# Performance work log

Measured on AMD Instinct MI355X. Metric: run time of the kernel, lower is better.

Reference implementation:

```python
import jax, jax.numpy as jnp
import numpy as np

B, T, C = 16, 512, 1024   # batch, frames, activation_dim
D = 4096                  # dict_size
K = 128                   # top-k per window
WIN = 8                   # window_size


def setup_inputs() -> dict:
    key = jax.random.key(0)
    k1, k2, k3, k4 = jax.random.split(key, 4)
    # decoder weight (C, D), columns normalized as in __init__
    W_dec = jax.random.normal(k1, (C, D), jnp.float32)
    W_dec = W_dec / jnp.linalg.norm(W_dec, axis=0, keepdims=True)
    # encoder initialized as decoder transpose (then independently perturbed to mimic training)
    W_enc = W_dec.T + 0.01 * jax.random.normal(k2, (D, C), jnp.float32)
    b_enc = 0.01 * jax.random.normal(k3, (D,), jnp.float32)
    b_dec = 0.01 * jax.random.normal(k4, (C,), jnp.float32)
    x = jax.random.normal(jax.random.fold_in(key, 7), (B, T, C), jnp.float32)
    return {"x": x, "W_enc": W_enc, "b_enc": b_enc, "W_dec": W_dec, "b_dec": b_dec}


def _window_topk(pre, k, win):
    # pre: (B, T, D) post-relu activations
    b, t, d = pre.shape
    pad = (-t) % win  # static
    if pad:
        pre_p = jnp.pad(pre, ((0, 0), (0, pad), (0, 0)))
    else:
        pre_p = pre
    tp = t + pad
    nw = tp // win
    xw = pre_p.reshape(b, nw, win, d)
    ws = xw.sum(axis=2)                        # (B, nw, D) window sums
    _, idx = jax.lax.top_k(ws, k)              # (B, nw, K)
    # scatter 1.0 at top-k dictionary entries per (batch, window) row
    idx_flat = idx.reshape(b * nw, k)
    rows = jnp.arange(b * nw)[:, None]
    mask = jnp.zeros((b * nw, d), pre.dtype).at[rows, idx_flat].set(1.0)
    mask = mask.reshape(b, nw, 1, d)
    sparse = (xw * mask).reshape(b, tp, d)[:, :t]
    return sparse


def reference(x, W_enc, b_enc, W_dec, b_dec):
    # encode: relu((x - b_dec) @ W_enc^T + b_enc)
    pre = jax.nn.relu(jnp.einsum('btc,dc->btd', x - b_dec, W_enc) + b_enc)  # (B,T,D)
    encoded = _window_topk(pre, K, WIN)                                     # (B,T,D)
    # decode: encoded @ W_dec^T + b_dec
    recon = jnp.einsum('btd,cd->btc', encoded, W_dec) + b_dec               # (B,T,C)
    return recon, encoded
```

## Files before the change

kernel.cpp:

```cpp
#include <hip/hip_runtime.h>

#define B_   16
#define T_   512
#define C_   1024
#define D_   4096
#define K_   128
#define WIN_ 8
#define NW_  (T_ / WIN_)
#define M_   (B_ * T_)

typedef __attribute__((ext_vector_type(8))) short bf16x8_t;
typedef __attribute__((ext_vector_type(4))) float f32x4_t;

__device__ __forceinline__ void gload16(const void* g, void* l) {
    __builtin_amdgcn_global_load_lds(
        (const __attribute__((address_space(1))) void*)g,
        (__attribute__((address_space(3))) void*)l, 16, 0, 0);
}

__device__ __forceinline__ unsigned short f2bf(float f) {
    unsigned u = __float_as_uint(f);
    unsigned r = (u + 0x7fffu + ((u >> 16) & 1u)) >> 16;
    return (unsigned short)r;
}
__device__ __forceinline__ float bf2f(unsigned short h) {
    return __uint_as_float((unsigned)h << 16);
}

__device__ __forceinline__ unsigned f2key(float f) {
    unsigned u = __float_as_uint(f);
    return (u & 0x80000000u) ? ~u : (u | 0x80000000u);
}
__device__ __forceinline__ float key2f(unsigned k) {
    unsigned u = (k & 0x80000000u) ? (k & 0x7fffffffu) : ~k;
    return __uint_as_float(u);
}

__global__ __launch_bounds__(256) void prep_cvt_wenc(
    const float* __restrict__ W_enc, const float* __restrict__ b_enc,
    const float* __restrict__ b_dec, unsigned short* __restrict__ wencbf,
    float* __restrict__ benc2)
{
    int d = blockIdx.x;
    int tid = threadIdx.x;
    float4 wv = ((const float4*)(W_enc + (size_t)d * C_))[tid];
    uint2 o;
    o.x = (unsigned)f2bf(wv.x) | ((unsigned)f2bf(wv.y) << 16);
    o.y = (unsigned)f2bf(wv.z) | ((unsigned)f2bf(wv.w) << 16);
    ((uint2*)(wencbf + (size_t)d * C_))[tid] = o;
    float4 bv = ((const float4*)b_dec)[tid];
    float s = wv.x * bv.x + wv.y * bv.y + wv.z * bv.z + wv.w * bv.w;
    __shared__ float red[256];
    red[tid] = s;
    __syncthreads();
    for (int off = 128; off > 0; off >>= 1) {
        if (tid < off) red[tid] += red[tid + off];
        __syncthreads();
    }
    if (tid == 0) benc2[d] = b_enc[d] - red[0];
}

__global__ void cvt_bf16(const float* __restrict__ in, unsigned short* __restrict__ out, int n8)
{
    int i = blockIdx.x * blockDim.x + threadIdx.x;
    if (i >= n8) return;
    const float4* p = (const float4*)(in + (size_t)i * 8);
    float4 a = p[0], b = p[1];
    uint4 o;
    o.x = (unsigned)f2bf(a.x) | ((unsigned)f2bf(a.y) << 16);
    o.y = (unsigned)f2bf(a.z) | ((unsigned)f2bf(a.w) << 16);
    o.z = (unsigned)f2bf(b.x) | ((unsigned)f2bf(b.y) << 16);
    o.w = (unsigned)f2bf(b.z) | ((unsigned)f2bf(b.w) << 16);
    ((uint4*)out)[i] = o;
}

__global__ void transpose_wdec(const float* __restrict__ W, unsigned short* __restrict__ WT)
{
    __shared__ float tile[32][33];
    int d0 = blockIdx.x * 32;
    int c0 = blockIdx.y * 32;
    int tx = threadIdx.x, ty = threadIdx.y;
    #pragma unroll
    for (int i = 0; i < 32; i += 8)
        tile[ty + i][tx] = W[(size_t)(c0 + ty + i) * D_ + d0 + tx];
    __syncthreads();
    #pragma unroll
    for (int i = 0; i < 32; i += 8)
        WT[(size_t)(d0 + ty + i) * C_ + c0 + tx] = f2bf(tile[tx][ty + i]);
}

__global__ __launch_bounds__(256) void mfma_gemm_dense(
    const unsigned short* __restrict__ Abf,
    const unsigned short* __restrict__ Bbf,
    const float* __restrict__ benc2,
    float* __restrict__ enc,
    float* __restrict__ wsums)
{
    __shared__ unsigned short lA[128 * 32];
    __shared__ unsigned short lB[128 * 32];
    __shared__ float cst[4][16][68];
    int tid = threadIdx.x;
    int lane = tid & 63;
    int wv = tid >> 6;
    int wm = wv >> 1, wn = wv & 1;

    int lid = blockIdx.y * gridDim.x + blockIdx.x;
    int sw = (lid & 7) * 256 + (lid >> 3);
    int bn = sw & 31, bm = sw >> 5;

    f32x4_t acc[4][4];
    #pragma unroll
    for (int i = 0; i < 4; i++)
        #pragma unroll
        for (int j = 0; j < 4; j++) acc[i][j] = (f32x4_t){0.f, 0.f, 0.f, 0.f};

    const unsigned short* Ab = Abf + (size_t)bm * 128 * C_;
    const unsigned short* Bb = Bbf + (size_t)bn * 128 * C_;

    int m_s[2], u_s[2];
    #pragma unroll
    for (int q = 0; q < 2; q++) {
        int p = q * 256 + tid;
        int m = p >> 2, v = p & 3;
        m_s[q] = m;
        u_s[q] = v ^ ((m >> 1) & 3);
    }

    int r = lane & 15, g = lane >> 4;
    for (int k0 = 0; k0 < C_; k0 += 32) {
        __syncthreads();
        #pragma unroll
        for (int q = 0; q < 2; q++) {
            gload16(Ab + (size_t)m_s[q] * C_ + k0 + u_s[q] * 8,
                    &lA[(q * 256 + wv * 64) * 8]);
            gload16(Bb + (size_t)m_s[q] * C_ + k0 + u_s[q] * 8,
                    &lB[(q * 256 + wv * 64) * 8]);
        }
        __syncthreads();
        bf16x8_t af[4], bfr[4];
        #pragma unroll
        for (int mi = 0; mi < 4; mi++) {
            int m = wm * 64 + mi * 16 + r;
            int u = g ^ ((m >> 1) & 3);
            af[mi] = *(const bf16x8_t*)&lA[m * 32 + u * 8];
        }
        #pragma unroll
        for (int ni = 0; ni < 4; ni++) {
            int d = wn * 64 + ni * 16 + r;
            int u = g ^ ((d >> 1) & 3);
            bfr[ni] = *(const bf16x8_t*)&lB[d * 32 + u * 8];
        }
        #pragma unroll
        for (int mi = 0; mi < 4; mi++)
            #pragma unroll
            for (int ni = 0; ni < 4; ni++)
                acc[mi][ni] = __builtin_amdgcn_mfma_f32_16x16x32_bf16(
                    af[mi], bfr[ni], acc[mi][ni], 0, 0, 0);
    }

    int b = bm >> 2;
    int t_blk = (bm & 3) * 128;
    int dbase = bn * 128 + wn * 64;
    int mbase_w = bm * 128 + wm * 64;
    int wbase = b * NW_ + (t_blk >> 3) + wm * 8;

    float bias_r[4];
    #pragma unroll
    for (int ni = 0; ni < 4; ni++) bias_r[ni] = benc2[dbase + ni * 16 + r];

    float wsv[4][4];
    #pragma unroll
    for (int mi = 0; mi < 4; mi++) {
        #pragma unroll
        for (int ni = 0; ni < 4; ni++) {
            float s = 0.f;
            #pragma unroll
            for (int q = 0; q < 4; q++) {
                float v = acc[mi][ni][q] + bias_r[ni];
                v = v > 0.f ? v : 0.f;
                cst[wv][g * 4 + q][ni * 16 + r] = v;
                s += v;
            }
            float partner = __shfl_xor(s, 16);
            wsv[mi][ni] = s + partner;
        }
        #pragma unroll
        for (int ri = 0; ri < 4; ri++) {
            int row = ri * 4 + (lane >> 4);
            int c4 = (lane & 15) * 4;
            float4 vv = *(const float4*)&cst[wv][row][c4];
            *(float4*)(enc + (size_t)(mbase_w + mi * 16 + row) * D_ + dbase + c4) = vv;
        }
    }

    if ((g & 1) == 0) {
        #pragma unroll
        for (int mi = 0; mi < 4; mi++)
            #pragma unroll
            for (int ni = 0; ni < 4; ni++)
                cst[wv][mi * 2 + (g >> 1)][ni * 16 + r] = wsv[mi][ni];
    }
    #pragma unroll
    for (int it = 0; it < 2; it++) {
        int row = lane >> 3;
        int c4 = (lane & 7) * 4 + it * 32;
        float4 vv = *(const float4*)&cst[wv][row][c4];
        *(float4*)(wsums + (size_t)(wbase + row) * D_ + dbase + c4) = vv;
    }
}

__device__ __forceinline__ void find_bucket(
    const int* hist, int need, int shift, unsigned pref,
    unsigned* shp, int* shn, int tid)
{
    if (tid < 64) {
        int L = tid;
        int h0 = hist[L * 4], h1 = hist[L * 4 + 1];
        int h2 = hist[L * 4 + 2], h3 = hist[L * 4 + 3];
        int s3 = h3, s2 = h2 + s3, s1 = h1 + s2, s0 = h0 + s1;
        int T = s0, I = T;
        #pragma unroll
        for (int off = 1; off < 64; off <<= 1) {
            int t = __shfl_down(I, off);
            if (L + off < 64) I += t;
        }
        int H = I - T;
        int S[5] = {H + s0, H + s1, H + s2, H + s3, H};
        #pragma unroll
        for (int j = 0; j < 4; j++) {
            if (S[j] >= need && S[j + 1] < need) {
                *shp = pref | ((unsigned)(L * 4 + j) << shift);
                *shn = need - S[j + 1];
            }
        }
    }
    __syncthreads();
}

__device__ __forceinline__ void radix_select(
    const unsigned* keys, int n, int need0, int npass, unsigned maxkey,
    int* hist, unsigned* shp, int* shn, int tid)
{
    if (tid == 0) { *shp = 0u; *shn = need0; }
    __syncthreads();
    for (int pass = 0; pass < npass; ++pass) {
        int shift = 24 - pass * 8;
        unsigned pref = *shp;
        int need = *shn;
        unsigned pmask = (pass == 0) ? 0u : (0xFFFFFFFFu << (shift + 8));
        hist[tid] = 0;
        __syncthreads();
        for (int i = tid; i < n; i += 256) {
            unsigned k = keys[i];
            if (k <= maxkey && (k & pmask) == pref)
                atomicAdd(&hist[(k >> shift) & 0xFF], 1);
        }
        __syncthreads();
        find_bucket(hist, need, shift, pref, shp, shn, tid);
    }
}

__device__ __forceinline__ int block_prefix_excl(int v, int* wsum, int tid)
{
    __syncthreads();
    int lane = tid & 63, wv = tid >> 6;
    int x = v;
    #pragma unroll
    for (int off = 1; off < 64; off <<= 1) {
        int t = __shfl_up(x, off);
        if (lane >= off) x += t;
    }
    if (lane == 63) wsum[wv] = x;
    __syncthreads();
    int base = 0;
    #pragma unroll
    for (int w2 = 0; w2 < 3; w2++) if (w2 < wv) base += wsum[w2];
    return base + x - v;
}

#define DELTA 0.15f
#define MAXCAND 320

__global__ __launch_bounds__(256) void fixup_topk(
    const float* __restrict__ wsums, const float* __restrict__ x,
    const float* __restrict__ W_enc, const float* __restrict__ benc2,
    unsigned* __restrict__ bmask, int* __restrict__ idxlist)
{
    int row = blockIdx.x;
    int b = row / NW_, w = row % NW_;
    int t0g = b * T_ + w * WIN_;
    __shared__ unsigned keys[D_];
    __shared__ float xs[WIN_][C_];
    __shared__ int hist[256];
    __shared__ int wsum[4];
    __shared__ unsigned sh_prefix;
    __shared__ int sh_need;
    __shared__ int cand[MAXCAND];
    __shared__ unsigned ckeys[MAXCAND];
    __shared__ int sh_ncand, sh_nhi;
    unsigned short* hbits = (unsigned short*)hist;
    int* whist = (int*)xs;
    int tid = threadIdx.x;

    for (int i = tid; i < D_ / 4; i += 256) {
        float4 v = ((const float4*)(wsums + (size_t)row * D_))[i];
        keys[i * 4 + 0] = f2key(v.x);
        keys[i * 4 + 1] = f2key(v.y);
        keys[i * 4 + 2] = f2key(v.z);
        keys[i * 4 + 3] = f2key(v.w);
    }
    for (int i = tid; i < 1024; i += 256) whist[i] = 0;
    if (tid == 0) { sh_ncand = 0; sh_nhi = 0; }
    __syncthreads();

    {
        int* myh = whist + (tid >> 6) * 256;
        for (int i = tid; i < D_; i += 256)
            atomicAdd(&myh[keys[i] >> 24], 1);
        __syncthreads();
        hist[tid] = whist[tid] + whist[256 + tid] + whist[512 + tid] + whist[768 + tid];
        __syncthreads();
        find_bucket(hist, K_, 24, 0u, &sh_prefix, &sh_need, tid);
    }
    for (int pass = 1; pass < 3; ++pass) {
        int shift = 24 - pass * 8;
        unsigned pref = sh_prefix;
        int need = sh_need;
        unsigned pmask = 0xFFFFFFFFu << (shift + 8);
        hist[tid] = 0;
        __syncthreads();
        for (int i = tid; i < D_; i += 256) {
            unsigned k = keys[i];
            if ((k & pmask) == pref)
                atomicAdd(&hist[(k >> shift) & 0xFF], 1);
        }
        __syncthreads();
        find_bucket(hist, need, shift, pref, &sh_prefix, &sh_need, tid);
    }
    float kthf = key2f(sh_prefix);
    unsigned TH_HI = f2key(kthf + DELTA);
    unsigned TH_LO = f2key(kthf - DELTA);

    for (int i = tid; i < WIN_ * C_ / 4; i += 256)
        ((float4*)xs)[i] = ((const float4*)(x + (size_t)t0g * C_))[i];
    {
        int myhi = 0;
        for (int i = tid; i < D_; i += 256) {
            unsigned k = keys[i];
            if (k > TH_HI) myhi++;
            else if (k >= TH_LO) {
                int pos = atomicAdd(&sh_ncand, 1);
                if (pos < MAXCAND) cand[pos] = i;
            }
        }
        if (myhi) atomicAdd(&sh_nhi, myhi);
    }
    __syncthreads();
    int nc = sh_ncand < MAXCAND ? sh_ncand : MAXCAND;

    {
        int wvi = tid >> 6, ln = tid & 63;
        int c0 = ln * 4;
        for (int cb = wvi; cb < nc; cb += 4) {
            int d = cand[cb];
            const float* wrow = W_enc + (size_t)d * C_;
            float a[WIN_] = {0.f, 0.f, 0.f, 0.f, 0.f, 0.f, 0.f, 0.f};
            #pragma unroll
            for (int q = 0; q < 4; q++) {
                float4 wq = *(const float4*)(wrow + q * 256 + c0);
                #pragma unroll
                for (int j = 0; j < WIN_; j++) {
                    float4 xq = *(const float4*)(&xs[j][q * 256 + c0]);
                    a[j] = fmaf(wq.x, xq.x, a[j]);
                    a[j] = fmaf(wq.y, xq.y, a[j]);
                    a[j] = fmaf(wq.z, xq.z, a[j]);
                    a[j] = fmaf(wq.w, xq.w, a[j]);
                }
            }
            #pragma unroll
            for (int off = 1; off < 64; off <<= 1)
                #pragma unroll
                for (int j = 0; j < WIN_; j++) a[j] += __shfl_xor(a[j], off);
            if (ln == 0) {
                float bias = benc2[d], s = 0.f;
                #pragma unroll
                for (int j = 0; j < WIN_; j++) {
                    float v = a[j] + bias;
                    s += v > 0.f ? v : 0.f;
                }
                unsigned k1 = f2key(s);
                keys[d] = k1;
                ckeys[cb] = k1;
            }
        }
    }
    __syncthreads();

    for (int i = tid; i < nc; i += 256)
        if (ckeys[i] > TH_HI) atomicAdd(&sh_nhi, 1);
    __syncthreads();
    int need0 = K_ - sh_nhi;
    if (need0 > 0)
        radix_select(ckeys, nc, need0, 4, TH_HI, hist, &sh_prefix, &sh_need, tid);
    else
        radix_select(keys, D_, K_, 4, 0xFFFFFFFFu, hist, &sh_prefix, &sh_need, tid);
    unsigned kth = sh_prefix;
    int need_eq = sh_need;

    int base16 = tid * 16;
    unsigned mybits = 0;
    int eqcnt = 0;
    #pragma unroll
    for (int j = 0; j < 16; ++j) {
        unsigned k = keys[base16 + j];
        if (k > kth) mybits |= (1u << j);
        else if (k == kth) eqcnt++;
    }
    int rr = block_prefix_excl(eqcnt, wsum, tid);
    #pragma unroll
    for (int j = 0; j < 16; ++j) {
        unsigned k = keys[base16 + j];
        if (k == kth) { if (rr < need_eq) mybits |= (1u << j); rr++; }
    }
    hbits[tid] = (unsigned short)mybits;
    __syncthreads();
    if (tid < D_ / 32)
        bmask[(size_t)row * (D_ / 32) + tid] =
            (unsigned)hbits[2 * tid] | ((unsigned)hbits[2 * tid + 1] << 16);

    int pos = block_prefix_excl(__popc(mybits), wsum, tid);
    #pragma unroll
    for (int j = 0; j < 16; ++j) {
        if (mybits & (1u << j)) idxlist[(size_t)row * K_ + pos++] = base16 + j;
    }
}

__global__ void apply_mask(float* __restrict__ enc, const unsigned* __restrict__ bmask)
{
    size_t idx = ((size_t)blockIdx.x * blockDim.x + threadIdx.x) * 4;
    size_t m = idx >> 12;
    int d = (int)(idx & (D_ - 1));
    int b = (int)(m / T_);
    int t = (int)(m % T_);
    int wrow = b * NW_ + (t >> 3);
    unsigned word = bmask[(size_t)wrow * (D_ / 32) + (d >> 5)];
    unsigned nib = (word >> (d & 31)) & 0xFu;
    float4 v = {0.f, 0.f, 0.f, 0.f};
    if (nib) {
        v = *(float4*)(enc + idx);
        if (!(nib & 1u)) v.x = 0.f;
        if (!(nib & 2u)) v.y = 0.f;
        if (!(nib & 4u)) v.z = 0.f;
        if (!(nib & 8u)) v.w = 0.f;
    }
    *(float4*)(enc + idx) = v;
}

__global__ __launch_bounds__(256) void decode_win(
    const float* __restrict__ enc,
    const int* __restrict__ idxlist,
    const unsigned short* __restrict__ WdTb,
    const float* __restrict__ b_dec,
    float* __restrict__ recon)
{
    int row = blockIdx.x;
    int b = row / NW_, w = row % NW_;
    int t0 = b * T_ + w * WIN_;
    __shared__ int sidx[K_];
    __shared__ float act[K_][12];
    int tid = threadIdx.x;
    if (tid < K_) sidx[tid] = idxlist[(size_t)row * K_ + tid];
    __syncthreads();
    {
        int ci = tid >> 1;
        int j4 = (tid & 1) * 4;
        int dd = sidx[ci];
        #pragma unroll
        for (int j = 0; j < 4; j++)
            act[ci][j4 + j] = enc[(size_t)(t0 + j4 + j) * D_ + dd];
    }
    __syncthreads();

    float accv[WIN_][4] = {};
    int c0 = tid * 4;
    for (int i = 0; i < K_; ++i) {
        int d = sidx[i];
        ushort4 wu = *(const ushort4*)(WdTb + (size_t)d * C_ + c0);
        float4 wv = {bf2f(wu.x), bf2f(wu.y), bf2f(wu.z), bf2f(wu.w)};
        float4 a03 = *(const float4*)(&act[i][0]);
        float4 a47 = *(const float4*)(&act[i][4]);
        float aj[8] = {a03.x, a03.y, a03.z, a03.w, a47.x, a47.y, a47.z, a47.w};
        #pragma unroll
        for (int j = 0; j < WIN_; j++) {
            accv[j][0] = fmaf(aj[j], wv.x, accv[j][0]);
            accv[j][1] = fmaf(aj[j], wv.y, accv[j][1]);
            accv[j][2] = fmaf(aj[j], wv.z, accv[j][2]);
            accv[j][3] = fmaf(aj[j], wv.w, accv[j][3]);
        }
    }
    float4 bd = *(const float4*)(b_dec + c0);
    #pragma unroll
    for (int j = 0; j < WIN_; j++) {
        float4 o;
        o.x = accv[j][0] + bd.x; o.y = accv[j][1] + bd.y;
        o.z = accv[j][2] + bd.z; o.w = accv[j][3] + bd.w;
        *(float4*)(recon + (size_t)(t0 + j) * C_ + c0) = o;
    }
}

extern "C" void kernel_launch(void* const* d_in, const int* in_sizes, int n_in,
                              void* d_out, int out_size, void* d_ws, size_t ws_size,
                              hipStream_t stream)
{
    const float* x     = (const float*)d_in[0];
    const float* W_enc = (const float*)d_in[1];
    const float* b_enc = (const float*)d_in[2];
    const float* W_dec = (const float*)d_in[3];
    const float* b_dec = (const float*)d_in[4];

    float* out   = (float*)d_out;
    float* recon = out;
    float* enc   = out + (size_t)M_ * C_;

    unsigned short* xbf   = (unsigned short*)recon;
    float*          wsums = (float*)((char*)recon + (size_t)M_ * C_ * 2);

    char* ws = (char*)d_ws;
    unsigned short* WdTb    = (unsigned short*)ws;
    unsigned*       bmask   = (unsigned*)(ws + (size_t)D_ * C_ * 4);
    int*            idxlist = (int*)((char*)bmask + (size_t)(B_ * NW_) * (D_ / 32) * 4);
    float*          benc2   = (float*)((char*)idxlist + (size_t)(B_ * NW_) * K_ * 4);
    unsigned short* wencbf  = (unsigned short*)((char*)benc2 + D_ * 4);

    prep_cvt_wenc<<<D_, 256, 0, stream>>>(W_enc, b_enc, b_dec, wencbf, benc2);
    cvt_bf16<<<(M_ * C_ / 8 + 255) / 256, 256, 0, stream>>>(x, xbf, M_ * C_ / 8);
    transpose_wdec<<<dim3(D_ / 32, C_ / 32), dim3(32, 8), 0, stream>>>(W_dec, WdTb);
    mfma_gemm_dense<<<dim3(32, 64), 256, 0, stream>>>(xbf, wencbf, benc2, enc, wsums);
    fixup_topk<<<B_ * NW_, 256, 0, stream>>>(wsums, x, W_enc, benc2, bmask, idxlist);
    apply_mask<<<(int)((size_t)M_ * D_ / 4 / 256), 256, 0, stream>>>(enc, bmask);
    decode_win<<<B_ * NW_, 256, 0, stream>>>(enc, idxlist, WdTb, b_dec, recon);
}
```

Baseline: 275.4 us.

## Fuse top-k fixup, mask application and window decode into one kernel

Merges the top-k selection, the dense mask-apply pass and the per-window decoder into a single per-window kernel. The bitmask and index list now stay in LDS instead of going through global memory, and the kept activations are gathered into LDS while the encoded rows are masked, which removes two launches and a re-read of the sparse values. The catch is that only 1024 blocks of 256 threads do the whole 128 MB enc read/write pass, which may limit memory bandwidth, and LDS regions are reused across phases.

```diff
diff --git a/kernel.cpp b/kernel.cpp
--- a/kernel.cpp
+++ b/kernel.cpp
@@ -281,10 +281,11 @@
 #define DELTA 0.15f
 #define MAXCAND 320
 
-__global__ __launch_bounds__(256) void fixup_topk(
+__global__ __launch_bounds__(256) void fixup_mask_decode(
     const float* __restrict__ wsums, const float* __restrict__ x,
     const float* __restrict__ W_enc, const float* __restrict__ benc2,
-    unsigned* __restrict__ bmask, int* __restrict__ idxlist)
+    const unsigned short* __restrict__ WdTb, const float* __restrict__ b_dec,
+    float* __restrict__ enc, float* __restrict__ recon)
 {
     int row = blockIdx.x;
     int b = row / NW_, w = row % NW_;
@@ -300,6 +301,10 @@
     __shared__ int sh_ncand, sh_nhi;
     unsigned short* hbits = (unsigned short*)hist;
     int* whist = (int*)xs;
+    float (*act)[12] = (float(*)[12])xs;
+    int*      sidx      = cand;
+    unsigned* bmask_lds = (unsigned*)(cand + 128);
+    int*      pprefix   = (int*)ckeys;
     int tid = threadIdx.x;
 
     for (int i = tid; i < D_ / 4; i += 256) {
@@ -424,87 +429,70 @@
     }
     hbits[tid] = (unsigned short)mybits;
     __syncthreads();
-    if (tid < D_ / 32)
-        bmask[(size_t)row * (D_ / 32) + tid] =
-            (unsigned)hbits[2 * tid] | ((unsigned)hbits[2 * tid + 1] << 16);
-
+    if (tid < 128)
+        bmask_lds[tid] = (unsigned)hbits[2 * tid] | ((unsigned)hbits[2 * tid + 1] << 16);
+    int pv = (tid < 128) ? __popc((unsigned)hbits[2 * tid] | ((unsigned)hbits[2 * tid + 1] << 16)) : 0;
+    int ppref = block_prefix_excl(pv, wsum, tid);
+    if (tid < 128) pprefix[tid] = ppref;
     int pos = block_prefix_excl(__popc(mybits), wsum, tid);
     #pragma unroll
     for (int j = 0; j < 16; ++j) {
-        if (mybits & (1u << j)) idxlist[(size_t)row * K_ + pos++] = base16 + j;
-    }
-}
-
-__global__ void apply_mask(float* __restrict__ enc, const unsigned* __restrict__ bmask)
-{
-    size_t idx = ((size_t)blockIdx.x * blockDim.x + threadIdx.x) * 4;
-    size_t m = idx >> 12;
-    int d = (int)(idx & (D_ - 1));
-    int b = (int)(m / T_);
-    int t = (int)(m % T_);
-    int wrow = b * NW_ + (t >> 3);
-    unsigned word = bmask[(size_t)wrow * (D_ / 32) + (d >> 5)];
-    unsigned nib = (word >> (d & 31)) & 0xFu;
-    float4 v = {0.f, 0.f, 0.f, 0.f};
-    if (nib) {
-        v = *(float4*)(enc + idx);
-        if (!(nib & 1u)) v.x = 0.f;
-        if (!(nib & 2u)) v.y = 0.f;
-        if (!(nib & 4u)) v.z = 0.f;
-        if (!(nib & 8u)) v.w = 0.f;
-    }
-    *(float4*)(enc + idx) = v;
-}
-
-__global__ __launch_bounds__(256) void decode_win(
-    const float* __restrict__ enc,
-    const int* __restrict__ idxlist,
-    const unsigned short* __restrict__ WdTb,
-    const float* __restrict__ b_dec,
-    float* __restrict__ recon)
-{
-    int row = blockIdx.x;
-    int b = row / NW_, w = row % NW_;
-    int t0 = b * T_ + w * WIN_;
-    __shared__ int sidx[K_];
-    __shared__ float act[K_][12];
-    int tid = threadIdx.x;
-    if (tid < K_) sidx[tid] = idxlist[(size_t)row * K_ + tid];
-    __syncthreads();
+        if (mybits & (1u << j)) sidx[pos++] = base16 + j;
+    }
+    __syncthreads();
+
+    for (int jrow = 0; jrow < WIN_; jrow++) {
+        float* rowp = enc + (size_t)(t0g + jrow) * D_;
+        #pragma unroll
+        for (int k4 = 0; k4 < 4; k4++) {
+            int d4 = tid + k4 * 256;
+            int widx = d4 >> 3;
+            int bit0 = (d4 & 7) * 4;
+            unsigned word = bmask_lds[widx];
+            unsigned nib = (word >> bit0) & 0xFu;
+            float4 v = {0.f, 0.f, 0.f, 0.f};
+            if (nib) {
+                v = ((const float4*)rowp)[d4];
+                int rk = pprefix[widx] + __popc(word & ((1u << bit0) - 1u));
+                float vals[4] = {v.x, v.y, v.z, v.w};
+                #pragma unroll
+                for (int l = 0; l < 4; l++) {
+                    if (nib & (1u << l)) { act[rk][jrow] = vals[l]; rk++; }
+                    else vals[l] = 0.f;
+                }
+                v.x = vals[0]; v.y = vals[1]; v.z = vals[2]; v.w = vals[3];
+            }
+            ((float4*)rowp)[d4] = v;
+        }
+    }
+    __syncthreads();
+
     {
-        int ci = tid >> 1;
-        int j4 = (tid & 1) * 4;
-        int dd = sidx[ci];
-        #pragma unroll
-        for (int j = 0; j < 4; j++)
-            act[ci][j4 + j] = enc[(size_t)(t0 + j4 + j) * D_ + dd];
-    }
-    __syncthreads();
-
-    float accv[WIN_][4] = {};
-    int c0 = tid * 4;
-    for (int i = 0; i < K_; ++i) {
-        int d = sidx[i];
-        ushort4 wu = *(const ushort4*)(WdTb + (size_t)d * C_ + c0);
-        float4 wv = {bf2f(wu.x), bf2f(wu.y), bf2f(wu.z), bf2f(wu.w)};
-        float4 a03 = *(const float4*)(&act[i][0]);
-        float4 a47 = *(const float4*)(&act[i][4]);
-        float aj[8] = {a03.x, a03.y, a03.z, a03.w, a47.x, a47.y, a47.z, a47.w};
+        float accv[WIN_][4] = {};
+        int c0 = tid * 4;
+        for (int i = 0; i < K_; ++i) {
+            int d = sidx[i];
+            ushort4 wu = *(const ushort4*)(WdTb + (size_t)d * C_ + c0);
+            float4 wv = {bf2f(wu.x), bf2f(wu.y), bf2f(wu.z), bf2f(wu.w)};
+            float4 a03 = *(const float4*)(&act[i][0]);
+            float4 a47 = *(const float4*)(&act[i][4]);
+            float aj[8] = {a03.x, a03.y, a03.z, a03.w, a47.x, a47.y, a47.z, a47.w};
+            #pragma unroll
+            for (int j = 0; j < WIN_; j++) {
+                accv[j][0] = fmaf(aj[j], wv.x, accv[j][0]);
+                accv[j][1] = fmaf(aj[j], wv.y, accv[j][1]);
+                accv[j][2] = fmaf(aj[j], wv.z, accv[j][2]);
+                accv[j][3] = fmaf(aj[j], wv.w, accv[j][3]);
+            }
+        }
+        float4 bd = *(const float4*)(b_dec + c0);
         #pragma unroll
         for (int j = 0; j < WIN_; j++) {
-            accv[j][0] = fmaf(aj[j], wv.x, accv[j][0]);
-            accv[j][1] = fmaf(aj[j], wv.y, accv[j][1]);
-            accv[j][2] = fmaf(aj[j], wv.z, accv[j][2]);
-            accv[j][3] = fmaf(aj[j], wv.w, accv[j][3]);
-        }
-    }
-    float4 bd = *(const float4*)(b_dec + c0);
-    #pragma unroll
-    for (int j = 0; j < WIN_; j++) {
-        float4 o;
-        o.x = accv[j][0] + bd.x; o.y = accv[j][1] + bd.y;
-        o.z = accv[j][2] + bd.z; o.w = accv[j][3] + bd.w;
-        *(float4*)(recon + (size_t)(t0 + j) * C_ + c0) = o;
+            float4 o;
+            o.x = accv[j][0] + bd.x; o.y = accv[j][1] + bd.y;
+            o.z = accv[j][2] + bd.z; o.w = accv[j][3] + bd.w;
+            *(float4*)(recon + (size_t)(t0g + j) * C_ + c0) = o;
+        }
     }
 }
 
@@ -527,16 +515,13 @@
 
     char* ws = (char*)d_ws;
     unsigned short* WdTb    = (unsigned short*)ws;
-    unsigned*       bmask   = (unsigned*)(ws + (size_t)D_ * C_ * 4);
-    int*            idxlist = (int*)((char*)bmask + (size_t)(B_ * NW_) * (D_ / 32) * 4);
-    float*          benc2   = (float*)((char*)idxlist + (size_t)(B_ * NW_) * K_ * 4);
+    float*          benc2   = (float*)(ws + (size_t)D_ * C_ * 2);
     unsigned short* wencbf  = (unsigned short*)((char*)benc2 + D_ * 4);
 
     prep_cvt_wenc<<<D_, 256, 0, stream>>>(W_enc, b_enc, b_dec, wencbf, benc2);
     cvt_bf16<<<(M_ * C_ / 8 + 255) / 256, 256, 0, stream>>>(x, xbf, M_ * C_ / 8);
     transpose_wdec<<<dim3(D_ / 32, C_ / 32), dim3(32, 8), 0, stream>>>(W_dec, WdTb);
     mfma_gemm_dense<<<dim3(32, 64), 256, 0, stream>>>(xbf, wencbf, benc2, enc, wsums);
-    fixup_topk<<<B_ * NW_, 256, 0, stream>>>(wsums, x, W_enc, benc2, bmask, idxlist);
-    apply_mask<<<(int)((size_t)M_ * D_ / 4 / 256), 256, 0, stream>>>(enc, bmask);
-    decode_win<<<B_ * NW_, 256, 0, stream>>>(enc, idxlist, WdTb, b_dec, recon);
-}
+    fixup_mask_decode<<<B_ * NW_, 256, 0, stream>>>(
+        wsums, x, W_enc, benc2, WdTb, b_dec, enc, recon);
+}
```

After: 276.9 us. About the same (+0.6%).
